# Performance work log

Measured on AMD Instinct MI355X. Metric: run time of the kernel, lower is better.

Reference implementation:

```python
import jax, jax.numpy as jnp
import numpy as np
import math

B, L, D, H = 2, 2048, 1024, 16

def setup_inputs() -> dict:
    key = jax.random.key(0)
    ks = jax.random.split(key, 5)
    return {
        "query": jax.random.normal(ks[0], (B, L, D), dtype=jnp.float32),
        "key": jax.random.normal(ks[1], (B, L, D), dtype=jnp.float32),
        "value": jax.random.normal(ks[2], (B, L, D), dtype=jnp.float32),
        "w_out": jax.random.normal(ks[3], (D, D), dtype=jnp.float32) * (1.0 / math.sqrt(D)),
        "b_out": jnp.zeros((D,), dtype=jnp.float32),
    }

def reference(query, key, value, w_out, b_out):
    b, l, d_model = query.shape
    num_heads = H
    head_dim = d_model // num_heads
    scaling = 1.0 / math.sqrt(d_model)  # NOTE: module scales by embed_dim, not head_dim

    def reshape(x):
        return x.reshape(b, l, num_heads, head_dim).transpose(0, 2, 1, 3)  # [B,H,L,hd]

    q, k, v = reshape(query), reshape(key), reshape(value)
    scores = jnp.einsum("bhqd,bhkd->bhqk", q, k) * scaling  # [B,H,L,L]

    u = max(1, int(math.ceil(math.log(l + 1))))  # static: 8 for L=2048
    _, topk_idx = jax.lax.top_k(scores, u)  # [B,H,L,u]

    # scatter True at top-u key positions per query
    bi = jnp.arange(b)[:, None, None, None]
    hi = jnp.arange(num_heads)[None, :, None, None]
    qi = jnp.arange(l)[None, None, :, None]
    mask = jnp.zeros(scores.shape, dtype=bool).at[bi, hi, qi, topk_idx].set(True)

    scores_masked = jnp.where(mask, scores, -jnp.inf)
    attn_weights = jax.nn.softmax(scores_masked, axis=-1)  # [B,H,L,L]

    attn_out = jnp.einsum("bhqk,bhkd->bhqd", attn_weights, v)
    attn_out = attn_out.transpose(0, 2, 1, 3).reshape(b, l, d_model)
    attn_out = attn_out @ w_out.T + b_out  # nn.Linear
    return attn_out, attn_weights
```

## Files before the change

### kernel.cpp

```cpp
#include <hip/hip_runtime.h>
#include <math.h>

#define BB 2
#define LL 2048
#define DD 1024
#define HH 16
#define SCALE 0.03125f

#define ATTN_ELEMS ((size_t)BB * LL * DD)

typedef unsigned short u16;
typedef __attribute__((ext_vector_type(8))) short bf16x8;
typedef __attribute__((ext_vector_type(4))) float f32x4;

__device__ __forceinline__ u16 f2bf_rne(float f) {
    union { float f; unsigned u; } c; c.f = f;
    unsigned u = c.u;
    u += 0x7fffu + ((u >> 16) & 1u);
    return (u16)(u >> 16);
}

__device__ __forceinline__ void splitbf(float x, short& h, short& l) {
    union { float f; unsigned u; } c; c.f = x;
    unsigned uh = c.u & 0xFFFF0000u;
    h = (short)(uh >> 16);
    union { unsigned u; float f; } ch; ch.u = uh;
    l = (short)f2bf_rne(x - ch.f);
}

__device__ __forceinline__ void insert8(float (&tv)[8], int (&ti)[8], float cv, int ci) {
    bool g0 = cv > tv[0], g1 = cv > tv[1], g2 = cv > tv[2], g3 = cv > tv[3],
         g4 = cv > tv[4], g5 = cv > tv[5], g6 = cv > tv[6];
    tv[7] = g6 ? tv[6] : cv;                 ti[7] = g6 ? ti[6] : ci;
    tv[6] = g5 ? tv[5] : (g6 ? cv : tv[6]);  ti[6] = g5 ? ti[5] : (g6 ? ci : ti[6]);
    tv[5] = g4 ? tv[4] : (g5 ? cv : tv[5]);  ti[5] = g4 ? ti[4] : (g5 ? ci : ti[5]);
    tv[4] = g3 ? tv[3] : (g4 ? cv : tv[4]);  ti[4] = g3 ? ti[3] : (g4 ? ci : ti[4]);
    tv[3] = g2 ? tv[2] : (g3 ? cv : tv[3]);  ti[3] = g2 ? ti[2] : (g3 ? ci : ti[3]);
    tv[2] = g1 ? tv[1] : (g2 ? cv : tv[2]);  ti[2] = g1 ? ti[1] : (g2 ? ci : ti[2]);
    tv[1] = g0 ? tv[0] : (g1 ? cv : tv[1]);  ti[1] = g0 ? ti[0] : (g1 ? ci : ti[1]);
    tv[0] = g0 ? cv : tv[0];                 ti[0] = g0 ? ci : ti[0];
}

__device__ __forceinline__ void merge4(
    const float* v0, const int* i0, const float* v1, const int* i1,
    const float* v2, const int* i2, const float* v3, const int* i3,
    float* ov, int* oi)
{
    int p0 = 0, p1 = 0, p2 = 0, p3 = 0;
    #pragma unroll
    for (int s = 0; s < 8; ++s) {
        float a0 = v0[p0], a1 = v1[p1], a2 = v2[p2], a3 = v3[p3];
        int   b0 = i0[p0], b1 = i1[p1], b2 = i2[p2], b3 = i3[p3];
        float bv = a0; int bi = b0; int bc = 0;
        if (a1 > bv || (a1 == bv && b1 < bi)) { bv = a1; bi = b1; bc = 1; }
        if (a2 > bv || (a2 == bv && b2 < bi)) { bv = a2; bi = b2; bc = 2; }
        if (a3 > bv || (a3 == bv && b3 < bi)) { bv = a3; bi = b3; bc = 3; }
        p0 += (bc == 0); p1 += (bc == 1); p2 += (bc == 2); p3 += (bc == 3);
        ov[s] = bv; oi[s] = bi;
    }
}

__global__ __launch_bounds__(256) void attn_kernel(
    const float* __restrict__ q, const float* __restrict__ k, const float* __restrict__ v,
    float* __restrict__ aw, float* __restrict__ ctx)
{
    const int bid  = blockIdx.x;
    const int qt   = bid & 31;
    const int h    = (bid >> 5) & 15;
    const int b    = bid >> 9;
    const int t    = threadIdx.x;
    const int wv   = t >> 6;
    const int lane = t & 63;
    const int li   = lane & 15;
    const int quad = lane >> 4;

    __shared__ __align__(16) char smA[32768];
    __shared__ float s2v[32][4][8];
    __shared__ int   s2i[32][4][8];
    __shared__ int   cidx[32][12];
    __shared__ float cs[32][12];
    __shared__ float wrow[64][8];
    __shared__ int   wix[64][8];
    u16* khi = (u16*)smA;
    u16* klo = (u16*)(smA + 16384);

    const float* kbase = k + ((size_t)b * LL) * DD + h * 64;
    f32x4* awz = (f32x4*)(aw + (((size_t)(b * HH + h) * LL) + (size_t)qt * 64) * LL);
    const f32x4 zero4 = {0.f, 0.f, 0.f, 0.f};

    bf16x8 qh0, ql0, qh1, ql1;
    {
        const float* qrow = q + ((size_t)(b * LL + qt * 64 + wv * 16 + li)) * DD + h * 64;
        float x[8];
        *(f32x4*)x       = *(const f32x4*)(qrow + quad * 8);
        *(f32x4*)(x + 4) = *(const f32x4*)(qrow + quad * 8 + 4);
        #pragma unroll
        for (int e = 0; e < 8; ++e) { short hh, ll; splitbf(x[e], hh, ll); qh0[e] = hh; ql0[e] = ll; }
        *(f32x4*)x       = *(const f32x4*)(qrow + 32 + quad * 8);
        *(f32x4*)(x + 4) = *(const f32x4*)(qrow + 32 + quad * 8 + 4);
        #pragma unroll
        for (int e = 0; e < 8; ++e) { short hh, ll; splitbf(x[e], hh, ll); qh1[e] = hh; ql1[e] = ll; }
    }

    float tv[4][8]; int tix[4][8];
    #pragma unroll
    for (int r = 0; r < 4; ++r)
        #pragma unroll
        for (int s = 0; s < 8; ++s) { tv[r][s] = -INFINITY; tix[r][s] = 0; }

    for (int iter = 0; iter < 16; ++iter) {
        __syncthreads();
        #pragma unroll
        for (int j = 0; j < 4; ++j) {
            int f   = j * 256 + t;
            int col = f >> 3;
            int c   = (f >> 2) & 1;
            int qd  = f & 3;
            const float* src = kbase + (size_t)(iter * 128 + col) * DD + c * 32 + qd * 8;
            float x[8];
            *(f32x4*)x       = *(const f32x4*)src;
            *(f32x4*)(x + 4) = *(const f32x4*)(src + 4);
            bf16x8 h8, l8;
            #pragma unroll
            for (int e = 0; e < 8; ++e) { short hh, ll; splitbf(x[e], hh, ll); h8[e] = hh; l8[e] = ll; }
            int off = (((col >> 4) * 2 + c) << 9) + (qd << 7) + ((col & 15) << 3);
            *(bf16x8*)&khi[off] = h8;
            *(bf16x8*)&klo[off] = l8;
        }
        #pragma unroll
        for (int i = 0; i < 8; ++i) awz[iter * 2048 + i * 256 + t] = zero4;
        __syncthreads();

        #pragma unroll
        for (int s = 0; s < 8; ++s) {
            int fo = s << 10;
            bf16x8 kh0 = *(bf16x8*)&khi[fo + (lane << 3)];
            bf16x8 kh1 = *(bf16x8*)&khi[fo + 512 + (lane << 3)];
            bf16x8 kl0 = *(bf16x8*)&klo[fo + (lane << 3)];
            bf16x8 kl1 = *(bf16x8*)&klo[fo + 512 + (lane << 3)];
            f32x4 c4 = {0.f, 0.f, 0.f, 0.f};
            c4 = __builtin_amdgcn_mfma_f32_16x16x32_bf16(qh0, kh0, c4, 0, 0, 0);
            c4 = __builtin_amdgcn_mfma_f32_16x16x32_bf16(qh1, kh1, c4, 0, 0, 0);
            c4 = __builtin_amdgcn_mfma_f32_16x16x32_bf16(qh0, kl0, c4, 0, 0, 0);
            c4 = __builtin_amdgcn_mfma_f32_16x16x32_bf16(qh1, kl1, c4, 0, 0, 0);
            c4 = __builtin_amdgcn_mfma_f32_16x16x32_bf16(ql0, kh0, c4, 0, 0, 0);
            c4 = __builtin_amdgcn_mfma_f32_16x16x32_bf16(ql1, kh1, c4, 0, 0, 0);
            int ci = iter * 128 + s * 16 + li;
            #pragma unroll
            for (int r = 0; r < 4; ++r) {
                float cv = c4[r] * SCALE;
                if (cv > tv[r][7]) insert8(tv[r], tix[r], cv, ci);
            }
        }
    }

    float* mv = (float*)smA;
    int*   mi = (int*)(smA + 16384);
    for (int bb = 0; bb < 2; ++bb) {
        __syncthreads();
        if ((wv >> 1) == bb) {
            int rl0 = (wv & 1) * 16 + quad * 4;
            #pragma unroll
            for (int r = 0; r < 4; ++r) {
                int base = (rl0 + r) * 128 + li * 8;
                #pragma unroll
                for (int s = 0; s < 8; ++s) { mv[base + s] = tv[r][s]; mi[base + s] = tix[r][s]; }
            }
        }
        __syncthreads();
        if (t < 128) {
            int rr = t >> 2, p = t & 3;
            int base = rr * 128 + p * 32;
            merge4(&mv[base], &mi[base], &mv[base + 8], &mi[base + 8],
                   &mv[base + 16], &mi[base + 16], &mv[base + 24], &mi[base + 24],
                   s2v[rr][p], s2i[rr][p]);
        }
        __syncthreads();
        if (t < 32) {
            int rr = t;
            int pp[4] = {0, 0, 0, 0};
            #pragma unroll
            for (int s = 0; s < 12; ++s) {
                float bv = -INFINITY; int bi = 0x7fffffff; int bc = 0;
                #pragma unroll
                for (int l = 0; l < 4; ++l) {
                    if (pp[l] < 8) {
                        float hv = s2v[rr][l][pp[l]]; int hi2 = s2i[rr][l][pp[l]];
                        if (hv > bv || (hv == bv && hi2 < bi)) { bv = hv; bi = hi2; bc = l; }
                    }
                }
                pp[bc] += 1;
                cidx[rr][s] = bi;
            }
        }
        __syncthreads();
        for (int task = t; task < 384; task += 256) {
            int row = task / 12, c = task - row * 12;
            const float* qp = q + ((size_t)(b * LL + qt * 64 + bb * 32 + row)) * DD + h * 64;
            const float* kp = k + ((size_t)(b * LL + cidx[row][c])) * DD + h * 64;
            float acc = 0.f;
            for (int d4 = 0; d4 < 16; ++d4) {
                f32x4 qa = *(const f32x4*)(qp + d4 * 4);
                f32x4 ka = *(const f32x4*)(kp + d4 * 4);
                acc = fmaf(qa[0], ka[0], acc);
                acc = fmaf(qa[1], ka[1], acc);
                acc = fmaf(qa[2], ka[2], acc);
                acc = fmaf(qa[3], ka[3], acc);
            }
            cs[row][c] = acc * SCALE;
        }
        __syncthreads();
        if (t < 32) {
            int rr = t;
            float vv[12]; int ii[12];
            #pragma unroll
            for (int c = 0; c < 12; ++c) { vv[c] = cs[rr][c]; ii[c] = cidx[rr][c]; }
            float fv[8]; int fi[8];
            #pragma unroll
            for (int s = 0; s < 8; ++s) {
                float bv = -INFINITY; int bi = 0x7fffffff; int bc = 0;
                #pragma unroll
                for (int c = 0; c < 12; ++c) {
                    if (vv[c] > bv || (vv[c] == bv && ii[c] < bi)) { bv = vv[c]; bi = ii[c]; bc = c; }
                }
                vv[bc] = -INFINITY;
                fv[s] = bv; fi[s] = bi;
            }
            float m = fv[0];
            float e0[8]; float sum = 0.f;
            #pragma unroll
            for (int s = 0; s < 8; ++s) { e0[s] = __expf(fv[s] - m); sum += e0[s]; }
            float inv = 1.0f / sum;
            int grow = bb * 32 + rr;
            float* awrow = aw + (((size_t)(b * HH + h) * LL) + (size_t)qt * 64 + grow) * LL;
            #pragma unroll
            for (int s = 0; s < 8; ++s) {
                float w8 = e0[s] * inv;
                awrow[fi[s]] = w8;
                wrow[grow][s] = w8; wix[grow][s] = fi[s];
            }
        }
    }
    __syncthreads();

    const float* vbase = v + ((size_t)b * LL) * DD + h * 64;
    #pragma unroll
    for (int i = 0; i < 4; ++i) {
        int id = i * 256 + t;
        int row = id >> 4, seg = id & 15;
        f32x4 acc = {0.f, 0.f, 0.f, 0.f};
        #pragma unroll
        for (int s = 0; s < 8; ++s) {
            float ws = wrow[row][s];
            f32x4 vvv = *(const f32x4*)(vbase + (size_t)wix[row][s] * DD + seg * 4);
            acc[0] = fmaf(ws, vvv[0], acc[0]);
            acc[1] = fmaf(ws, vvv[1], acc[1]);
            acc[2] = fmaf(ws, vvv[2], acc[2]);
            acc[3] = fmaf(ws, vvv[3], acc[3]);
        }
        *(f32x4*)(ctx + ((size_t)(b * LL + qt * 64 + row)) * DD + h * 64 + seg * 4) = acc;
    }
}

__global__ __launch_bounds__(256) void linear_ws_kernel(
    const float* __restrict__ ctx, const float* __restrict__ w,
    const float* __restrict__ bias, float* __restrict__ out)
{
    const int bid  = blockIdx.x;
    const int nb   = bid & 15, mb = bid >> 4;
    const int t    = threadIdx.x;
    const int wv   = t >> 6;
    const int lane = t & 63;
    const int li   = lane & 15;
    const int quad = lane >> 4;

    __shared__ u16 bhi[8192], blo[8192];

    f32x4 acc0 = {0.f,0.f,0.f,0.f}, acc1 = {0.f,0.f,0.f,0.f},
          acc2 = {0.f,0.f,0.f,0.f}, acc3 = {0.f,0.f,0.f,0.f};
    const float* arow = ctx + (size_t)(mb * 64 + wv * 16 + li) * DD;

    for (int kc = 0; kc < 8; ++kc) {
        __syncthreads();
        #pragma unroll
        for (int j = 0; j < 4; ++j) {
            int f   = j * 256 + t;
            int col = f >> 4;
            int c   = (f >> 2) & 3;
            int qd  = f & 3;
            const float* src = w + (size_t)(nb * 64 + col) * DD + kc * 128 + c * 32 + qd * 8;
            float x[8];
            *(f32x4*)x       = *(const f32x4*)src;
            *(f32x4*)(x + 4) = *(const f32x4*)(src + 4);
            bf16x8 h8, l8;
            #pragma unroll
            for (int e = 0; e < 8; ++e) { short hh, ll; splitbf(x[e], hh, ll); h8[e] = hh; l8[e] = ll; }
            int off = (((col >> 4) * 4 + c) << 9) + (qd << 7) + ((col & 15) << 3);
            *(bf16x8*)&bhi[off] = h8;
            *(bf16x8*)&blo[off] = l8;
        }
        __syncthreads();

        bf16x8 ah[4], al[4];
        #pragma unroll
        for (int c = 0; c < 4; ++c) {
            float x[8];
            *(f32x4*)x       = *(const f32x4*)(arow + kc * 128 + c * 32 + quad * 8);
            *(f32x4*)(x + 4) = *(const f32x4*)(arow + kc * 128 + c * 32 + quad * 8 + 4);
            #pragma unroll
            for (int e = 0; e < 8; ++e) { short hh, ll; splitbf(x[e], hh, ll); ah[c][e] = hh; al[c][e] = ll; }
        }
        #pragma unroll
        for (int c = 0; c < 4; ++c) {
            bf16x8 bh0 = *(bf16x8*)&bhi[(( 0 + c) << 9) + (lane << 3)];
            bf16x8 bl0 = *(bf16x8*)&blo[(( 0 + c) << 9) + (lane << 3)];
            bf16x8 bh1 = *(bf16x8*)&bhi[(( 4 + c) << 9) + (lane << 3)];
            bf16x8 bl1 = *(bf16x8*)&blo[(( 4 + c) << 9) + (lane << 3)];
            bf16x8 bh2 = *(bf16x8*)&bhi[(( 8 + c) << 9) + (lane << 3)];
            bf16x8 bl2 = *(bf16x8*)&blo[(( 8 + c) << 9) + (lane << 3)];
            bf16x8 bh3 = *(bf16x8*)&bhi[((12 + c) << 9) + (lane << 3)];
            bf16x8 bl3 = *(bf16x8*)&blo[((12 + c) << 9) + (lane << 3)];
            acc0 = __builtin_amdgcn_mfma_f32_16x16x32_bf16(ah[c], bh0, acc0, 0, 0, 0);
            acc0 = __builtin_amdgcn_mfma_f32_16x16x32_bf16(ah[c], bl0, acc0, 0, 0, 0);
            acc0 = __builtin_amdgcn_mfma_f32_16x16x32_bf16(al[c], bh0, acc0, 0, 0, 0);
            acc1 = __builtin_amdgcn_mfma_f32_16x16x32_bf16(ah[c], bh1, acc1, 0, 0, 0);
            acc1 = __builtin_amdgcn_mfma_f32_16x16x32_bf16(ah[c], bl1, acc1, 0, 0, 0);
            acc1 = __builtin_amdgcn_mfma_f32_16x16x32_bf16(al[c], bh1, acc1, 0, 0, 0);
            acc2 = __builtin_amdgcn_mfma_f32_16x16x32_bf16(ah[c], bh2, acc2, 0, 0, 0);
            acc2 = __builtin_amdgcn_mfma_f32_16x16x32_bf16(ah[c], bl2, acc2, 0, 0, 0);
            acc2 = __builtin_amdgcn_mfma_f32_16x16x32_bf16(al[c], bh2, acc2, 0, 0, 0);
            acc3 = __builtin_amdgcn_mfma_f32_16x16x32_bf16(ah[c], bh3, acc3, 0, 0, 0);
            acc3 = __builtin_amdgcn_mfma_f32_16x16x32_bf16(ah[c], bl3, acc3, 0, 0, 0);
            acc3 = __builtin_amdgcn_mfma_f32_16x16x32_bf16(al[c], bh3, acc3, 0, 0, 0);
        }
    }

    #pragma unroll
    for (int st = 0; st < 4; ++st) {
        f32x4 a = (st == 0) ? acc0 : (st == 1) ? acc1 : (st == 2) ? acc2 : acc3;
        int col = nb * 64 + st * 16 + li;
        float bb2 = bias[col];
        #pragma unroll
        for (int r = 0; r < 4; ++r)
            out[(size_t)(mb * 64 + wv * 16 + quad * 4 + r) * DD + col] = a[r] + bb2;
    }
}

__global__ __launch_bounds__(256) void linear_inplace_kernel(
    float* io, const float* __restrict__ w, const float* __restrict__ bias)
{
    __shared__ u16 ahi[16384], alo[16384];
    const int t    = threadIdx.x;
    const int m0   = blockIdx.x * 16;
    const int wv   = t >> 6;
    const int lane = t & 63;
    const int li   = lane & 15;
    const int quad = lane >> 4;

    #pragma unroll
    for (int i = 0; i < 8; ++i) {
        int id  = i * 256 + t;
        int row = id >> 7;
        int c   = (id >> 2) & 31;
        int qd  = id & 3;
        const float* src = io + (size_t)(m0 + row) * DD + c * 32 + qd * 8;
        float x[8];
        *(f32x4*)x       = *(const f32x4*)src;
        *(f32x4*)(x + 4) = *(const f32x4*)(src + 4);
        bf16x8 h8, l8;
        #pragma unroll
        for (int e = 0; e < 8; ++e) { short hh, ll; splitbf(x[e], hh, ll); h8[e] = hh; l8[e] = ll; }
        int off = (c << 9) + (qd << 7) + (row << 3);
        *(bf16x8*)&ahi[off] = h8;
        *(bf16x8*)&alo[off] = l8;
    }
    __syncthreads();

    f32x4 acc[16];
    #pragma unroll
    for (int i = 0; i < 16; ++i) acc[i] = (f32x4){0.f, 0.f, 0.f, 0.f};

    for (int c = 0; c < 32; ++c) {
        bf16x8 ah = *(bf16x8*)&ahi[(c << 9) + (lane << 3)];
        bf16x8 al = *(bf16x8*)&alo[(c << 9) + (lane << 3)];
        #pragma unroll
        for (int sub = 0; sub < 16; ++sub) {
            int col = wv * 256 + sub * 16 + li;
            const float* src = w + (size_t)col * DD + c * 32 + quad * 8;
            float x[8];
            *(f32x4*)x       = *(const f32x4*)src;
            *(f32x4*)(x + 4) = *(const f32x4*)(src + 4);
            bf16x8 bh, bl;
            #pragma unroll
            for (int e = 0; e < 8; ++e) { short hh, ll; splitbf(x[e], hh, ll); bh[e] = hh; bl[e] = ll; }
            acc[sub] = __builtin_amdgcn_mfma_f32_16x16x32_bf16(ah, bh, acc[sub], 0, 0, 0);
            acc[sub] = __builtin_amdgcn_mfma_f32_16x16x32_bf16(ah, bl, acc[sub], 0, 0, 0);
            acc[sub] = __builtin_amdgcn_mfma_f32_16x16x32_bf16(al, bh, acc[sub], 0, 0, 0);
        }
    }

    #pragma unroll
    for (int sub = 0; sub < 16; ++sub) {
        int col = wv * 256 + sub * 16 + li;
        float bb2 = bias[col];
        #pragma unroll
        for (int r = 0; r < 4; ++r)
            io[(size_t)(m0 + quad * 4 + r) * DD + col] = acc[sub][r] + bb2;
    }
}

extern "C" void kernel_launch(void* const* d_in, const int* in_sizes, int n_in,
                              void* d_out, int out_size, void* d_ws, size_t ws_size,
                              hipStream_t stream) {
    const float* q    = (const float*)d_in[0];
    const float* k    = (const float*)d_in[1];
    const float* v    = (const float*)d_in[2];
    const float* w    = (const float*)d_in[3];
    const float* bias = (const float*)d_in[4];

    float* out = (float*)d_out;
    float* aw  = out + ATTN_ELEMS;

    const bool use_ws = (d_ws != nullptr) && (ws_size >= ATTN_ELEMS * sizeof(float));
    float* ctx = use_ws ? (float*)d_ws : out;

    attn_kernel<<<BB * HH * (LL / 64), 256, 0, stream>>>(q, k, v, aw, ctx);
    if (use_ws) {
        linear_ws_kernel<<<(BB * LL / 64) * (DD / 64), 256, 0, stream>>>(ctx, w, bias, out);
    } else {
        linear_inplace_kernel<<<BB * LL / 16, 256, 0, stream>>>(out, w, bias);
    }
}
```

Measured before the change: 887.1 us.

## Pre-split K and W into MFMA-ready bf16 hi/lo layouts in workspace

Adds prep kernels that split K and the output weight into bf16 hi/lo pairs stored in the fragment order MFMA expects. A new attention kernel streams these pre-laid-out K fragments straight from global memory with register double-buffering, instead of staging and converting through shared memory. It refines the top-8 candidates with an exact fp32 recheck of 12 candidates per row. The context is written as bf16 hi/lo so the linear kernel can feed MFMA directly, at the cost of extra workspace, two extra launches and more global traffic for the split copies.

```diff
diff --git a/kernel.cpp b/kernel.cpp
--- a/kernel.cpp
+++ b/kernel.cpp
@@ -11,6 +11,7 @@
 
 typedef unsigned short u16;
 typedef __attribute__((ext_vector_type(8))) short bf16x8;
+typedef __attribute__((ext_vector_type(4))) short s16x4;
 typedef __attribute__((ext_vector_type(4))) float f32x4;
 
 __device__ __forceinline__ u16 f2bf_rne(float f) {
@@ -59,6 +60,305 @@
         ov[s] = bv; oi[s] = bi;
     }
 }
+
+
+__global__ __launch_bounds__(256) void prep_k_kernel(
+    const float* __restrict__ k, u16* __restrict__ khi, u16* __restrict__ klo)
+{
+    int gid = blockIdx.x * 256 + threadIdx.x;
+    int li   = gid & 15;
+    int qd   = (gid >> 4) & 3;
+    int c    = (gid >> 6) & 1;
+    int s    = (gid >> 7) & 127;
+    int head = gid >> 14;
+    int b = head >> 4, h = head & 15;
+    const float* src = k + ((size_t)(b * LL + s * 16 + li)) * DD + h * 64 + c * 32 + qd * 8;
+    float x[8];
+    *(f32x4*)x       = *(const f32x4*)src;
+    *(f32x4*)(x + 4) = *(const f32x4*)(src + 4);
+    bf16x8 h8, l8;
+    #pragma unroll
+    for (int e = 0; e < 8; ++e) { short hh, ll; splitbf(x[e], hh, ll); h8[e] = hh; l8[e] = ll; }
+    *(bf16x8*)&khi[(size_t)gid * 8] = h8;
+    *(bf16x8*)&klo[(size_t)gid * 8] = l8;
+}
+
+__global__ __launch_bounds__(256) void prep_w_kernel(
+    const float* __restrict__ w, u16* __restrict__ whi, u16* __restrict__ wlo)
+{
+    int gid = blockIdx.x * 256 + threadIdx.x;
+    int li = gid & 15;
+    int qd = (gid >> 4) & 3;
+    int c  = (gid >> 6) & 3;
+    int nt = (gid >> 8) & 3;
+    int kc = (gid >> 10) & 7;
+    int nb = gid >> 13;
+    const float* src = w + (size_t)(nb * 64 + nt * 16 + li) * DD + kc * 128 + c * 32 + qd * 8;
+    float x[8];
+    *(f32x4*)x       = *(const f32x4*)src;
+    *(f32x4*)(x + 4) = *(const f32x4*)(src + 4);
+    bf16x8 h8, l8;
+    #pragma unroll
+    for (int e = 0; e < 8; ++e) { short hh, ll; splitbf(x[e], hh, ll); h8[e] = hh; l8[e] = ll; }
+    *(bf16x8*)&whi[(size_t)gid * 8] = h8;
+    *(bf16x8*)&wlo[(size_t)gid * 8] = l8;
+}
+
+__global__ __launch_bounds__(256) void attn_fast_kernel(
+    const float* __restrict__ q, const float* __restrict__ k, const float* __restrict__ v,
+    const u16* __restrict__ khi_g, const u16* __restrict__ klo_g,
+    float* __restrict__ aw, u16* __restrict__ chi, u16* __restrict__ clo)
+{
+    const int bid  = blockIdx.x;
+    const int qt   = bid & 31;
+    const int h    = (bid >> 5) & 15;
+    const int b    = bid >> 9;
+    const int t    = threadIdx.x;
+    const int wv   = t >> 6;
+    const int lane = t & 63;
+    const int li   = lane & 15;
+    const int quad = lane >> 4;
+
+    __shared__ float mv[4096];
+    __shared__ int   mi[4096];
+    __shared__ float s2v[32][4][8];
+    __shared__ int   s2i[32][4][8];
+    __shared__ int   cidx[32][12];
+    __shared__ float cs[32][12];
+    __shared__ float wrow[64][8];
+    __shared__ int   wix[64][8];
+
+    f32x4* awz = (f32x4*)(aw + (((size_t)(b * HH + h) * LL) + (size_t)qt * 64) * LL);
+    const f32x4 zero4 = {0.f, 0.f, 0.f, 0.f};
+
+    bf16x8 qh0, ql0, qh1, ql1;
+    {
+        const float* qrow = q + ((size_t)(b * LL + qt * 64 + wv * 16 + li)) * DD + h * 64;
+        float x[8];
+        *(f32x4*)x       = *(const f32x4*)(qrow + quad * 8);
+        *(f32x4*)(x + 4) = *(const f32x4*)(qrow + quad * 8 + 4);
+        #pragma unroll
+        for (int e = 0; e < 8; ++e) { short hh, ll; splitbf(x[e], hh, ll); qh0[e] = hh; ql0[e] = ll; }
+        *(f32x4*)x       = *(const f32x4*)(qrow + 32 + quad * 8);
+        *(f32x4*)(x + 4) = *(const f32x4*)(qrow + 32 + quad * 8 + 4);
+        #pragma unroll
+        for (int e = 0; e < 8; ++e) { short hh, ll; splitbf(x[e], hh, ll); qh1[e] = hh; ql1[e] = ll; }
+    }
+
+    float tv[4][8]; int tix[4][8];
+    #pragma unroll
+    for (int r = 0; r < 4; ++r)
+        #pragma unroll
+        for (int s = 0; s < 8; ++s) { tv[r][s] = -INFINITY; tix[r][s] = 0; }
+
+    const u16* khb = khi_g + (size_t)(b * HH + h) * 131072 + (size_t)lane * 8;
+    const u16* klb = klo_g + (size_t)(b * HH + h) * 131072 + (size_t)lane * 8;
+
+    bf16x8 kh0 = *(const bf16x8*)(khb);
+    bf16x8 kh1 = *(const bf16x8*)(khb + 512);
+    bf16x8 kl0 = *(const bf16x8*)(klb);
+    bf16x8 kl1 = *(const bf16x8*)(klb + 512);
+
+    #pragma unroll 2
+    for (int s = 0; s < 128; ++s) {
+        const int sn = (s + 1) & 127;
+        bf16x8 nh0 = *(const bf16x8*)(khb + (size_t)sn * 1024);
+        bf16x8 nh1 = *(const bf16x8*)(khb + (size_t)sn * 1024 + 512);
+        bf16x8 nl0 = *(const bf16x8*)(klb + (size_t)sn * 1024);
+        bf16x8 nl1 = *(const bf16x8*)(klb + (size_t)sn * 1024 + 512);
+
+        awz[s * 256 + t] = zero4;
+
+        f32x4 c4a = {0.f, 0.f, 0.f, 0.f};
+        f32x4 c4b = {0.f, 0.f, 0.f, 0.f};
+        c4a = __builtin_amdgcn_mfma_f32_16x16x32_bf16(qh0, kh0, c4a, 0, 0, 0);
+        c4b = __builtin_amdgcn_mfma_f32_16x16x32_bf16(qh1, kh1, c4b, 0, 0, 0);
+        c4a = __builtin_amdgcn_mfma_f32_16x16x32_bf16(qh0, kl0, c4a, 0, 0, 0);
+        c4b = __builtin_amdgcn_mfma_f32_16x16x32_bf16(qh1, kl1, c4b, 0, 0, 0);
+        c4a = __builtin_amdgcn_mfma_f32_16x16x32_bf16(ql0, kh0, c4a, 0, 0, 0);
+        c4b = __builtin_amdgcn_mfma_f32_16x16x32_bf16(ql1, kh1, c4b, 0, 0, 0);
+
+        int ci = s * 16 + li;
+        #pragma unroll
+        for (int r = 0; r < 4; ++r) {
+            float cv = (c4a[r] + c4b[r]) * SCALE;
+            if (cv > tv[r][7]) insert8(tv[r], tix[r], cv, ci);
+        }
+        kh0 = nh0; kh1 = nh1; kl0 = nl0; kl1 = nl1;
+    }
+
+    for (int bb = 0; bb < 2; ++bb) {
+        __syncthreads();
+        if ((wv >> 1) == bb) {
+            int rl0 = (wv & 1) * 16 + quad * 4;
+            #pragma unroll
+            for (int r = 0; r < 4; ++r) {
+                int base = (rl0 + r) * 128 + li * 8;
+                #pragma unroll
+                for (int s = 0; s < 8; ++s) { mv[base + s] = tv[r][s]; mi[base + s] = tix[r][s]; }
+            }
+        }
+        __syncthreads();
+        if (t < 128) {
+            int rr = t >> 2, p = t & 3;
+            int base = rr * 128 + p * 32;
+            merge4(&mv[base], &mi[base], &mv[base + 8], &mi[base + 8],
+                   &mv[base + 16], &mi[base + 16], &mv[base + 24], &mi[base + 24],
+                   s2v[rr][p], s2i[rr][p]);
+        }
+        __syncthreads();
+        if (t < 32) {
+            int rr = t;
+            int pp[4] = {0, 0, 0, 0};
+            #pragma unroll
+            for (int s = 0; s < 12; ++s) {
+                float bv = -INFINITY; int bi = 0x7fffffff; int bc = 0;
+                #pragma unroll
+                for (int l = 0; l < 4; ++l) {
+                    if (pp[l] < 8) {
+                        float hv = s2v[rr][l][pp[l]]; int hi2 = s2i[rr][l][pp[l]];
+                        if (hv > bv || (hv == bv && hi2 < bi)) { bv = hv; bi = hi2; bc = l; }
+                    }
+                }
+                pp[bc] += 1;
+                cidx[rr][s] = bi;
+            }
+        }
+        __syncthreads();
+        for (int task = t; task < 384; task += 256) {
+            int row = task / 12, c = task - row * 12;
+            const float* qp = q + ((size_t)(b * LL + qt * 64 + bb * 32 + row)) * DD + h * 64;
+            const float* kp = k + ((size_t)(b * LL + cidx[row][c])) * DD + h * 64;
+            float acc = 0.f;
+            for (int d4 = 0; d4 < 16; ++d4) {
+                f32x4 qa = *(const f32x4*)(qp + d4 * 4);
+                f32x4 ka = *(const f32x4*)(kp + d4 * 4);
+                acc = fmaf(qa[0], ka[0], acc);
+                acc = fmaf(qa[1], ka[1], acc);
+                acc = fmaf(qa[2], ka[2], acc);
+                acc = fmaf(qa[3], ka[3], acc);
+            }
+            cs[row][c] = acc * SCALE;
+        }
+        __syncthreads();
+        if (t < 32) {
+            int rr = t;
+            float vv[12]; int ii[12];
+            #pragma unroll
+            for (int c = 0; c < 12; ++c) { vv[c] = cs[rr][c]; ii[c] = cidx[rr][c]; }
+            float fv[8]; int fi[8];
+            #pragma unroll
+            for (int s = 0; s < 8; ++s) {
+                float bv = -INFINITY; int bi = 0x7fffffff; int bc = 0;
+                #pragma unroll
+                for (int c = 0; c < 12; ++c) {
+                    if (vv[c] > bv || (vv[c] == bv && ii[c] < bi)) { bv = vv[c]; bi = ii[c]; bc = c; }
+                }
+                vv[bc] = -INFINITY;
+                fv[s] = bv; fi[s] = bi;
+            }
+            float m = fv[0];
+            float e0[8]; float sum = 0.f;
+            #pragma unroll
+            for (int s = 0; s < 8; ++s) { e0[s] = __expf(fv[s] - m); sum += e0[s]; }
+            float inv = 1.0f / sum;
+            int grow = bb * 32 + rr;
+            float* awrow = aw + (((size_t)(b * HH + h) * LL) + (size_t)qt * 64 + grow) * LL;
+            #pragma unroll
+            for (int s = 0; s < 8; ++s) {
+                float w8 = e0[s] * inv;
+                awrow[fi[s]] = w8;
+                wrow[grow][s] = w8; wix[grow][s] = fi[s];
+            }
+        }
+    }
+    __syncthreads();
+
+    const float* vbase = v + ((size_t)b * LL) * DD + h * 64;
+    #pragma unroll
+    for (int i = 0; i < 4; ++i) {
+        int id = i * 256 + t;
+        int row = id >> 4, seg = id & 15;
+        f32x4 acc = {0.f, 0.f, 0.f, 0.f};
+        #pragma unroll
+        for (int s = 0; s < 8; ++s) {
+            float ws = wrow[row][s];
+            f32x4 vvv = *(const f32x4*)(vbase + (size_t)wix[row][s] * DD + seg * 4);
+            acc[0] = fmaf(ws, vvv[0], acc[0]);
+            acc[1] = fmaf(ws, vvv[1], acc[1]);
+            acc[2] = fmaf(ws, vvv[2], acc[2]);
+            acc[3] = fmaf(ws, vvv[3], acc[3]);
+        }
+        size_t off = ((size_t)(b * LL + qt * 64 + row)) * DD + h * 64 + seg * 4;
+        s16x4 h4, l4;
+        #pragma unroll
+        for (int j = 0; j < 4; ++j) { short hh, ll; splitbf(acc[j], hh, ll); h4[j] = hh; l4[j] = ll; }
+        *(s16x4*)(chi + off) = h4;
+        *(s16x4*)(clo + off) = l4;
+    }
+}
+
+__global__ __launch_bounds__(256) void linear_fast_kernel(
+    const u16* __restrict__ chi, const u16* __restrict__ clo,
+    const u16* __restrict__ whi, const u16* __restrict__ wlo,
+    const float* __restrict__ bias, float* __restrict__ out)
+{
+    const int bid  = blockIdx.x;
+    const int nb   = bid & 15, mb = bid >> 4;
+    const int t    = threadIdx.x;
+    const int wv   = t >> 6;
+    const int lane = t & 63;
+    const int li   = lane & 15;
+    const int quad = lane >> 4;
+
+    f32x4 acc0 = {0.f,0.f,0.f,0.f}, acc1 = {0.f,0.f,0.f,0.f},
+          acc2 = {0.f,0.f,0.f,0.f}, acc3 = {0.f,0.f,0.f,0.f};
+
+    const u16* ah_row = chi + (size_t)(mb * 64 + wv * 16 + li) * DD + quad * 8;
+    const u16* al_row = clo + (size_t)(mb * 64 + wv * 16 + li) * DD + quad * 8;
+    const size_t wboff = (size_t)nb * 65536 + (size_t)lane * 8;
+
+    for (int kc = 0; kc < 8; ++kc) {
+        const u16* wb_h = whi + wboff + kc * 8192;
+        const u16* wb_l = wlo + wboff + kc * 8192;
+        #pragma unroll
+        for (int c = 0; c < 4; ++c) {
+            bf16x8 ah = *(const bf16x8*)(ah_row + kc * 128 + c * 32);
+            bf16x8 al = *(const bf16x8*)(al_row + kc * 128 + c * 32);
+            bf16x8 bh0 = *(const bf16x8*)(wb_h + c * 512);
+            bf16x8 bl0 = *(const bf16x8*)(wb_l + c * 512);
+            bf16x8 bh1 = *(const bf16x8*)(wb_h + 2048 + c * 512);
+            bf16x8 bl1 = *(const bf16x8*)(wb_l + 2048 + c * 512);
+            bf16x8 bh2 = *(const bf16x8*)(wb_h + 4096 + c * 512);
+            bf16x8 bl2 = *(const bf16x8*)(wb_l + 4096 + c * 512);
+            bf16x8 bh3 = *(const bf16x8*)(wb_h + 6144 + c * 512);
+            bf16x8 bl3 = *(const bf16x8*)(wb_l + 6144 + c * 512);
+            acc0 = __builtin_amdgcn_mfma_f32_16x16x32_bf16(ah, bh0, acc0, 0, 0, 0);
+            acc0 = __builtin_amdgcn_mfma_f32_16x16x32_bf16(ah, bl0, acc0, 0, 0, 0);
+            acc0 = __builtin_amdgcn_mfma_f32_16x16x32_bf16(al, bh0, acc0, 0, 0, 0);
+            acc1 = __builtin_amdgcn_mfma_f32_16x16x32_bf16(ah, bh1, acc1, 0, 0, 0);
+            acc1 = __builtin_amdgcn_mfma_f32_16x16x32_bf16(ah, bl1, acc1, 0, 0, 0);
+            acc1 = __builtin_amdgcn_mfma_f32_16x16x32_bf16(al, bh1, acc1, 0, 0, 0);
+            acc2 = __builtin_amdgcn_mfma_f32_16x16x32_bf16(ah, bh2, acc2, 0, 0, 0);
+            acc2 = __builtin_amdgcn_mfma_f32_16x16x32_bf16(ah, bl2, acc2, 0, 0, 0);
+            acc2 = __builtin_amdgcn_mfma_f32_16x16x32_bf16(al, bh2, acc2, 0, 0, 0);
+            acc3 = __builtin_amdgcn_mfma_f32_16x16x32_bf16(ah, bh3, acc3, 0, 0, 0);
+            acc3 = __builtin_amdgcn_mfma_f32_16x16x32_bf16(ah, bl3, acc3, 0, 0, 0);
+            acc3 = __builtin_amdgcn_mfma_f32_16x16x32_bf16(al, bh3, acc3, 0, 0, 0);
+        }
+    }
+
+    #pragma unroll
+    for (int st = 0; st < 4; ++st) {
+        f32x4 a = (st == 0) ? acc0 : (st == 1) ? acc1 : (st == 2) ? acc2 : acc3;
+        int col = nb * 64 + st * 16 + li;
+        float bb2 = bias[col];
+        #pragma unroll
+        for (int r = 0; r < 4; ++r)
+            out[(size_t)(mb * 64 + wv * 16 + quad * 4 + r) * DD + col] = a[r] + bb2;
+    }
+}
+
 
 __global__ __launch_bounds__(256) void attn_kernel(
     const float* __restrict__ q, const float* __restrict__ k, const float* __restrict__ v,
@@ -421,13 +721,30 @@
     float* out = (float*)d_out;
     float* aw  = out + ATTN_ELEMS;
 
-    const bool use_ws = (d_ws != nullptr) && (ws_size >= ATTN_ELEMS * sizeof(float));
-    float* ctx = use_ws ? (float*)d_ws : out;
-
-    attn_kernel<<<BB * HH * (LL / 64), 256, 0, stream>>>(q, k, v, aw, ctx);
-    if (use_ws) {
-        linear_ws_kernel<<<(BB * LL / 64) * (DD / 64), 256, 0, stream>>>(ctx, w, bias, out);
+    const size_t CHI_ELE = ATTN_ELEMS;
+    const size_t KSP_ELE = 4194304;
+    const size_t WSP_ELE = 1048576;
+    const size_t need_fast = (2 * CHI_ELE + 2 * KSP_ELE + 2 * WSP_ELE) * sizeof(u16);
+
+    if (d_ws != nullptr && ws_size >= need_fast) {
+        u16* chi = (u16*)d_ws;
+        u16* clo = chi + CHI_ELE;
+        u16* khi = clo + CHI_ELE;
+        u16* klo = khi + KSP_ELE;
+        u16* whi = klo + KSP_ELE;
+        u16* wlo = whi + WSP_ELE;
+        prep_k_kernel<<<2048, 256, 0, stream>>>(k, khi, klo);
+        prep_w_kernel<<<512, 256, 0, stream>>>(w, whi, wlo);
+        attn_fast_kernel<<<BB * HH * (LL / 64), 256, 0, stream>>>(q, k, v, khi, klo, aw, chi, clo);
+        linear_fast_kernel<<<(BB * LL / 64) * (DD / 64), 256, 0, stream>>>(chi, clo, whi, wlo, bias, out);
     } else {
-        linear_inplace_kernel<<<BB * LL / 16, 256, 0, stream>>>(out, w, bias);
-    }
-}
+        const bool use_ws = (d_ws != nullptr) && (ws_size >= ATTN_ELEMS * sizeof(float));
+        float* ctx = use_ws ? (float*)d_ws : out;
+        attn_kernel<<<BB * HH * (LL / 64), 256, 0, stream>>>(q, k, v, aw, ctx);
+        if (use_ws) {
+            linear_ws_kernel<<<(BB * LL / 64) * (DD / 64), 256, 0, stream>>>(ctx, w, bias, out);
+        } else {
+            linear_inplace_kernel<<<BB * LL / 16, 256, 0, stream>>>(out, w, bias);
+        }
+    }
+}
```

Result: no change. 886.6 us (-0.1%).
